# Kernel tuning notes

Measured on AMD Instinct MI355X. Metric: run time of the kernel, lower is better.

## Reference

```python
import jax, jax.numpy as jnp
import numpy as np

N = 4096   # number of observations
Q = 1024   # number of spatial locations (dist_matrix side)


def setup_inputs() -> dict:
    key = jax.random.key(0)
    k1, k2, k3, k4 = jax.random.split(key, 4)
    y_true = jax.random.normal(k1, (N, 1), dtype=jnp.float32)
    y_pred = jax.random.normal(k2, (N, 1), dtype=jnp.float32)
    Z_idx = jax.random.randint(k3, (N, 1), 0, Q).astype(jnp.int64)
    # symmetric distance matrix from random 2D coordinates
    coords = jax.random.uniform(k4, (Q, 2), dtype=jnp.float32) * 10.0
    diff = coords[:, None, :] - coords[None, :, :]
    dist_matrix = jnp.sqrt(jnp.sum(diff * diff, axis=-1) + 1e-12)
    sig2e = jnp.asarray(1.0, dtype=jnp.float32)
    sig2bs = jnp.ones((2,), dtype=jnp.float32)
    return {"y_true": y_true, "y_pred": y_pred, "Z_idx": Z_idx,
            "dist_matrix": dist_matrix, "sig2e": sig2e, "sig2bs": sig2bs}


def reference(y_true, y_pred, Z_idx, dist_matrix, sig2e, sig2bs):
    # NLL for the 'spatial' mixed-effects mode (custom_loss_lm).
    # V = sig2e*I + Z D Z^T with Z the one-hot indicator of Z_idx and
    # D[a,b] = sig2bs[0]*exp(-dist[a,b]/(2*sig2bs[1])).
    # Z D Z^T for one-hot Z is simply the row/col gather D[idx][:, idx],
    # which avoids materializing the dense N x Q indicator matrix.
    n = y_true.shape[0]
    idx = Z_idx[:, 0]
    D = sig2bs[0] * jnp.exp(-dist_matrix / (2.0 * sig2bs[1]))   # (Q, Q)
    V = sig2e * jnp.eye(n, dtype=jnp.float32) + D[idx][:, idx]  # (N, N)
    r = y_true - y_pred                                          # (N, 1)
    V_inv_r = jnp.linalg.solve(V, r)                             # (N, 1)
    quad = jnp.sum(r * V_inv_r)
    _, logdet = jnp.linalg.slogdet(V)
    log2pi = jnp.asarray(np.log(2.0 * np.pi), dtype=jnp.float32)
    total_loss = 0.5 * n * log2pi + 0.5 * logdet + 0.5 * quad
    return total_loss
```

## Files before the change

kernel.cpp:

```cpp
#include <hip/hip_runtime.h>
#include <math.h>

#define NN 4096
#define QQ 1024
#define LDA 1032
#define AF (1025 * 1032)


__device__ __forceinline__ void potrf64_run(float (&x)[16], int i, int q,
                                            float2 (&col2)[2][64]) {
#pragma unroll
    for (int qk = 0; qk < 4; ++qk) {
#pragma unroll
        for (int c2 = 0; c2 < 8; ++c2) {
            const int k = qk * 16 + 2 * c2;
            const int ck = 2 * c2;
            const int b = c2 & 1;
            if (q == qk) {
                float xk = x[ck];
                float d0 = __shfl(xk, k, 64);
                float rs0 = rsqrtf(d0);
                float l0 = (i == k) ? d0 * rs0 : xk * rs0;
                if (i >= k) x[ck] = l0;
                float lk1 = __shfl(l0, k + 1, 64);
                float x1v = fmaf(-l0, lk1, x[ck + 1]);
                float d1 = __shfl(x1v, k + 1, 64);
                float rs1 = rsqrtf(d1);
                float l1 = (i == k + 1) ? d1 * rs1 : x1v * rs1;
                if (i >= k + 1) x[ck + 1] = l1;
                col2[b][i] = make_float2(l0, l1);
            }
            __syncthreads();
            if (16 * q + 15 > k + 1 && i > k) {
                float2 lp = col2[b][i];
                const float4* cp = (const float4*)(&col2[b][16 * q]);
#pragma unroll
                for (int m2 = 0; m2 < 8; ++m2) {
                    float4 v = cp[m2];
                    if (16 * q + 2 * m2 > k + 1)
                        x[2 * m2] = fmaf(-lp.x, v.x, fmaf(-lp.y, v.y, x[2 * m2]));
                    if (16 * q + 2 * m2 + 1 > k + 1)
                        x[2 * m2 + 1] = fmaf(-lp.x, v.z, fmaf(-lp.y, v.w, x[2 * m2 + 1]));
                }
            }
        }
    }
}

template<bool DUAL>
__device__ __forceinline__ void trsm64_fused(float* Tr, float* Tc,
                                             const float (&Lb)[64][65],
                                             const float (&dinv)[64],
                                             float2 (&colr)[2][64],
                                             float2 (&colc)[2][64]) {
    const int tid = threadIdx.x;
    const int r = tid & 63, q = tid >> 6;
    float* tpr = Tr + r * 68 + 16 * q;
    float* tpc = Tc + r * 68 + 16 * q;
    float xr[16], xc[16];
#pragma unroll
    for (int m4 = 0; m4 < 4; ++m4) {
        float4 v = ((const float4*)tpr)[m4];
        xr[4 * m4] = v.x; xr[4 * m4 + 1] = v.y; xr[4 * m4 + 2] = v.z; xr[4 * m4 + 3] = v.w;
        if (DUAL) {
            float4 u = ((const float4*)tpc)[m4];
            xc[4 * m4] = u.x; xc[4 * m4 + 1] = u.y; xc[4 * m4 + 2] = u.z; xc[4 * m4 + 3] = u.w;
        }
    }
    float dv[16], ls[8];
#pragma unroll
    for (int m = 0; m < 16; ++m) dv[m] = dinv[16 * q + m];
#pragma unroll
    for (int c2 = 0; c2 < 8; ++c2) ls[c2] = Lb[16 * q + 2 * c2 + 1][16 * q + 2 * c2];
#pragma unroll
    for (int qk = 0; qk < 4; ++qk) {
#pragma unroll
        for (int c2 = 0; c2 < 8; ++c2) {
            const int k = qk * 16 + 2 * c2;
            const int ck = 2 * c2;
            const int b = c2 & 1;
            if (q == qk) {
                float l0 = xr[ck] * dv[ck];
                xr[ck] = l0;
                float l1 = fmaf(-l0, ls[c2], xr[ck + 1]) * dv[ck + 1];
                xr[ck + 1] = l1;
                colr[b][r] = make_float2(l0, l1);
                if (DUAL) {
                    float m0 = xc[ck] * dv[ck];
                    xc[ck] = m0;
                    float m1 = fmaf(-m0, ls[c2], xc[ck + 1]) * dv[ck + 1];
                    xc[ck + 1] = m1;
                    colc[b][r] = make_float2(m0, m1);
                }
            }
            __syncthreads();
            if (16 * q + 15 > k + 1) {
                float2 lr = colr[b][r];
                float2 lc;
                if (DUAL) lc = colc[b][r];
#pragma unroll
                for (int m2 = 0; m2 < 8; ++m2) {
                    const int c0 = 16 * q + 2 * m2;
                    if (c0 > k + 1) {
                        float a0 = Lb[c0][k], a1 = Lb[c0][k + 1];
                        xr[2 * m2] = fmaf(-lr.x, a0, fmaf(-lr.y, a1, xr[2 * m2]));
                        if (DUAL)
                            xc[2 * m2] = fmaf(-lc.x, a0, fmaf(-lc.y, a1, xc[2 * m2]));
                    }
                    if (c0 + 1 > k + 1) {
                        float b0 = Lb[c0 + 1][k], b1 = Lb[c0 + 1][k + 1];
                        xr[2 * m2 + 1] = fmaf(-lr.x, b0, fmaf(-lr.y, b1, xr[2 * m2 + 1]));
                        if (DUAL)
                            xc[2 * m2 + 1] = fmaf(-lc.x, b0, fmaf(-lc.y, b1, xc[2 * m2 + 1]));
                    }
                }
            }
        }
    }
#pragma unroll
    for (int m4 = 0; m4 < 4; ++m4) {
        ((float4*)tpr)[m4] = make_float4(xr[4 * m4], xr[4 * m4 + 1],
                                         xr[4 * m4 + 2], xr[4 * m4 + 3]);
        if (DUAL)
            ((float4*)tpc)[m4] = make_float4(xc[4 * m4], xc[4 * m4 + 1],
                                             xc[4 * m4 + 2], xc[4 * m4 + 3]);
    }
    __syncthreads();
}

__device__ __forceinline__ void panel_tile(
    float* __restrict__ A, float* __restrict__ scal, int p, int by, int bx,
    int nr, int ncol, float (&PrRaw)[64 * 68], float (&PcRaw)[64 * 68],
    float2 (&col2)[2][64], float2 (&colc)[2][64],
    float (&Lb)[64][65], float (&dinv)[64]) {
    const int tid = threadIdx.x;
    const int lane = tid & 63, wid = tid >> 6;
    int t0v = (p + 1) * 64;
    int r0 = t0v + by * 64;
    int c0 = t0v + bx * 64;
    bool wrow = (by == nr - 1);
    bool same_rc = (bx == by) && !wrow;
    bool dfuse = (bx == 0 && by == 0);
    int pc0 = p * 64;
    const float* db = A + (size_t)pc0 * (LDA + 1);
    for (int idx2 = tid; idx2 < 1024; idx2 += 256) {
        int rr = idx2 >> 4, c4 = idx2 & 15;
        int gr = r0 + rr;
        float4 v = make_float4(0.f, 0.f, 0.f, 0.f);
        if (gr <= QQ) v = *(const float4*)(A + (size_t)gr * LDA + pc0 + 4 * c4);
        *(float4*)(PrRaw + rr * 68 + 4 * c4) = v;
        if (!same_rc) {
            float4 u = *(const float4*)(A + (size_t)(c0 + rr) * LDA + pc0 + 4 * c4);
            *(float4*)(PcRaw + rr * 68 + 4 * c4) = u;
        }
    }
    for (int kk = tid; kk < 4096; kk += 256) {
        int ii = kk >> 6, jj = kk & 63;
        Lb[ii][jj] = db[(size_t)ii * LDA + jj];
    }
    if (tid < 64) dinv[tid] = 1.0f / db[(size_t)tid * (LDA + 1)];
    __syncthreads();
    if (same_rc) trsm64_fused<false>(PrRaw, PcRaw, Lb, dinv, col2, colc);
    else         trsm64_fused<true >(PrRaw, PcRaw, Lb, dinv, col2, colc);
    if (wrow && bx == 0 && wid == 0) {
        float xv = PrRaw[lane];
        float v = xv * xv;
        for (int o = 32; o > 0; o >>= 1) v += __shfl_down(v, o, 64);
        if (lane == 0) atomicAdd(&scal[2], v);
    }
    const float* PB = same_rc ? PrRaw : PcRaw;
    int tx = tid & 15, ty = tid >> 4;
    float acc[4][4];
#pragma unroll
    for (int ii = 0; ii < 4; ++ii)
#pragma unroll
        for (int jj = 0; jj < 4; ++jj) acc[ii][jj] = 0.f;
    float4 ar4[4], br4[4];
#pragma unroll 4
    for (int k4 = 0; k4 < 16; ++k4) {
#pragma unroll
        for (int ii = 0; ii < 4; ++ii)
            ar4[ii] = *(const float4*)(PrRaw + (ty + 16 * ii) * 68 + 4 * k4);
#pragma unroll
        for (int jj = 0; jj < 4; ++jj)
            br4[jj] = *(const float4*)(PB + (tx + 16 * jj) * 68 + 4 * k4);
#pragma unroll
        for (int ii = 0; ii < 4; ++ii)
#pragma unroll
            for (int jj = 0; jj < 4; ++jj) {
                acc[ii][jj] = fmaf(ar4[ii].x, br4[jj].x, acc[ii][jj]);
                acc[ii][jj] = fmaf(ar4[ii].y, br4[jj].y, acc[ii][jj]);
                acc[ii][jj] = fmaf(ar4[ii].z, br4[jj].z, acc[ii][jj]);
                acc[ii][jj] = fmaf(ar4[ii].w, br4[jj].w, acc[ii][jj]);
            }
    }
    if (!dfuse) {
#pragma unroll
        for (int ii = 0; ii < 4; ++ii) {
            int rr = r0 + ty + 16 * ii;
            if (rr <= QQ) {
#pragma unroll
                for (int jj = 0; jj < 4; ++jj) {
                    float* pa = A + (size_t)rr * LDA + c0 + tx + 16 * jj;
                    *pa -= acc[ii][jj];
                }
            }
        }
    } else {
#pragma unroll
        for (int ii = 0; ii < 4; ++ii) {
            int lr = ty + 16 * ii;
#pragma unroll
            for (int jj = 0; jj < 4; ++jj) {
                int lc = tx + 16 * jj;
                float old = A[(size_t)(r0 + lr) * LDA + c0 + lc];
                PcRaw[lr * 65 + lc] = old - acc[ii][jj];
            }
        }
        __syncthreads();
        int i = tid & 63, q = tid >> 6;
        float x[16];
#pragma unroll
        for (int m = 0; m < 16; ++m) x[m] = PcRaw[i * 65 + 16 * q + m];
        potrf64_run(x, i, q, col2);
        float* row = A + (size_t)(r0 + i) * LDA + c0 + 16 * q;
#pragma unroll
        for (int m4 = 0; m4 < 4; ++m4)
            ((float4*)row)[m4] = make_float4(x[4 * m4], x[4 * m4 + 1],
                                             x[4 * m4 + 2], x[4 * m4 + 3]);
    }
}

__global__ __launch_bounds__(256) void k_front(
    const float* __restrict__ yt, const float* __restrict__ yp,
    const int* __restrict__ idx, const float* __restrict__ dist,
    const float* __restrict__ se_p, const float* __restrict__ sbs,
    float* __restrict__ A, float* __restrict__ scal) {
    const int bid = blockIdx.x, tid = threadIdx.x;
    const int lane = tid & 63, wid = tid >> 6;
    __shared__ int   c_l[1024];
    __shared__ float s_l[1024];
    __shared__ float sq_l[1024];
    __shared__ __align__(16) float Pc[64 * 65];
    __shared__ float2 col2[2][64];
    __shared__ float red[4];
    float sb0 = sbs[0];
    float inv2 = 1.0f / (2.0f * sbs[1]);
    float inv_se = 1.0f / se_p[0];
    bool mv = (bid >= 128);

    for (int j = tid; j < 1024; j += 256) { c_l[j] = 0; s_l[j] = 0.f; }
    __syncthreads();
    float rr_acc = 0.f;
#pragma unroll
    for (int e4 = 0; e4 < 16; ++e4) {
        int e = tid + 256 * e4;
        int q = idx[e];
        atomicAdd(&c_l[q], 1);
        if (mv) {
            float r = yt[e] - yp[e];
            atomicAdd(&s_l[q], r);
            rr_acc += r * r;
        }
    }
    __syncthreads();
    for (int j = tid; j < 1024; j += 256) sq_l[j] = sqrtf((float)c_l[j]);
    __syncthreads();

    if (bid == 0) {
        for (int kk = tid; kk < 4096; kk += 256) {
            int i = kk >> 6, j = kk & 63;
            float qi = sq_l[i] * inv_se * sb0;
            Pc[i * 65 + j] = ((i == j) ? 1.0f : 0.0f)
                           + qi * sq_l[j] * __expf(-dist[(size_t)i * QQ + j] * inv2);
        }
        __syncthreads();
        int i = lane, q = wid;
        float x[16];
#pragma unroll
        for (int m = 0; m < 16; ++m) x[m] = Pc[i * 65 + 16 * q + m];
        potrf64_run(x, i, q, col2);
        float* row = A + (size_t)i * LDA + 16 * q;
#pragma unroll
        for (int m4 = 0; m4 < 4; ++m4)
            ((float4*)row)[m4] = make_float4(x[4 * m4], x[4 * m4 + 1],
                                             x[4 * m4 + 2], x[4 * m4 + 3]);
        if (tid == 0) scal[2] = 0.f;
    } else if (!mv) {
        for (int i = 64 + (bid - 1); i < QQ; i += 127) {
            float qi = sq_l[i] * inv_se * sb0;
            float4 d = ((const float4*)(dist + (size_t)i * QQ))[tid];
            int j0 = 4 * tid;
            float4 o;
            o.x = ((i == j0    ) ? 1.0f : 0.0f) + qi * sq_l[j0    ] * __expf(-d.x * inv2);
            o.y = ((i == j0 + 1) ? 1.0f : 0.0f) + qi * sq_l[j0 + 1] * __expf(-d.y * inv2);
            o.z = ((i == j0 + 2) ? 1.0f : 0.0f) + qi * sq_l[j0 + 2] * __expf(-d.z * inv2);
            o.w = ((i == j0 + 3) ? 1.0f : 0.0f) + qi * sq_l[j0 + 3] * __expf(-d.w * inv2);
            ((float4*)(A + (size_t)i * LDA))[tid] = o;
        }
    } else {
        int m = bid - 128;
        if (bid == 128) {
            float v = rr_acc;
            for (int o = 32; o > 0; o >>= 1) v += __shfl_down(v, o, 64);
            if (lane == 0) red[wid] = v;
            __syncthreads();
            if (tid == 0) scal[0] = red[0] + red[1] + red[2] + red[3];
            __syncthreads();
        }
        float st_acc = 0.f;
#pragma unroll
        for (int h = 0; h < 2; ++h) {
            int row = m * 8 + wid * 2 + h;
            const float* dr = dist + (size_t)row * QQ;
            float acc = 0.f;
#pragma unroll
            for (int j4 = 0; j4 < 16; ++j4) {
                int j = lane + 64 * j4;
                acc += __expf(-dr[j] * inv2) * s_l[j];
            }
            for (int o = 32; o > 0; o >>= 1) acc += __shfl_down(acc, o, 64);
            if (lane == 0) {
                float tv = acc * sb0;
                A[(size_t)QQ * LDA + row] = sq_l[row] * tv;
                st_acc += s_l[row] * tv;
            }
        }
        __syncthreads();
        if (lane == 0) red[wid] = st_acc;
        __syncthreads();
        if (tid == 0) scal[16 + m] = red[0] + red[1] + red[2] + red[3];
    }
}

__global__ __launch_bounds__(256) void k_panel(float* __restrict__ A,
                                               float* __restrict__ scal, int p) {
    __shared__ __align__(16) float PrRaw[64 * 68];
    __shared__ __align__(16) float PcRaw[64 * 68];
    __shared__ float2 col2[2][64];
    __shared__ float2 colc[2][64];
    __shared__ float Lb[64][65];
    __shared__ float dinv[64];
    int t0v = (p + 1) * 64;
    int rows = (QQ + 1) - t0v;
    int nr = (rows + 63) >> 6;
    int ncol = (QQ - t0v) / 64;
    int by = -1, bx = 0, rem = blockIdx.x;
    for (int b = 0; b < nr; ++b) {
        int cn = (b + 1 < ncol) ? (b + 1) : ncol;
        if (cn < 1) cn = 1;
        if (rem < cn) { by = b; bx = rem; break; }
        rem -= cn;
    }
    if (by < 0) return;
    panel_tile(A, scal, p, by, bx, nr, ncol, PrRaw, PcRaw, col2, colc, Lb, dinv);
}

__global__ __launch_bounds__(256) void k_final(float* __restrict__ A,
                                               float* __restrict__ scal,
                                               const float* __restrict__ se_p,
                                               float* __restrict__ out) {
    const int tid = threadIdx.x;
    const int lane = tid & 63, wid = tid >> 6;
    __shared__ float Lb[64][65];
    __shared__ float r1s[4], r2s[4], r3s[4];
    __shared__ float wl[64];
    const float* db15 = A + (size_t)960 * LDA + 960;
    for (int kk = tid; kk < 4096; kk += 256) {
        int ii = kk >> 6, jj = kk & 63;
        Lb[ii][jj] = db15[(size_t)ii * LDA + jj];
    }
    __syncthreads();
    if (tid < 64) {
        float xv = A[(size_t)QQ * LDA + 960 + tid];
        for (int k = 0; k < 64; ++k) {
            if (tid == k) xv /= Lb[k][k];
            float xk = __shfl(xv, k, 64);
            if (tid > k) xv = fmaf(-Lb[tid][k], xk, xv);
        }
        wl[tid] = xv;
    }
    __syncthreads();
    float v1 = 0.f, v2 = 0.f;
    for (int i = tid; i < QQ; i += 256) {
        v1 += __logf(A[(size_t)i * LDA + i]);
        if (i >= 960) { float yv = wl[i - 960]; v2 += yv * yv; }
    }
    v1 *= 2.0f;
    float v3 = (tid < 128) ? scal[16 + tid] : 0.f;
    for (int o = 32; o > 0; o >>= 1) {
        v1 += __shfl_down(v1, o, 64);
        v2 += __shfl_down(v2, o, 64);
        v3 += __shfl_down(v3, o, 64);
    }
    if (lane == 0) { r1s[wid] = v1; r2s[wid] = v2; r3s[wid] = v3; }
    __syncthreads();
    if (tid == 0) {
        float ld = r1s[0] + r1s[1] + r1s[2] + r1s[3];
        float wsq = __hip_atomic_load(&scal[2], __ATOMIC_RELAXED, __HIP_MEMORY_SCOPE_AGENT);
        float yy = r2s[0] + r2s[1] + r2s[2] + r2s[3] + wsq;
        float st = r3s[0] + r3s[1] + r3s[2] + r3s[3];
        float se = se_p[0], inv = 1.0f / se;
        float rr = scal[0];
        float quad = rr * inv - inv * inv * (st - inv * yy);
        float logdetV = (float)NN * __logf(se) + ld;
        out[0] = 0.5f * (float)NN * 1.8378770664093453f + 0.5f * logdetV + 0.5f * quad;
    }
}

extern "C" void kernel_launch(void* const* d_in, const int* in_sizes, int n_in,
                              void* d_out, int out_size, void* d_ws, size_t ws_size,
                              hipStream_t stream) {
    const float* yt   = (const float*)d_in[0];
    const float* yp   = (const float*)d_in[1];
    const int*   idx  = (const int*)d_in[2];
    const float* dist = (const float*)d_in[3];
    const float* se   = (const float*)d_in[4];
    const float* sbs  = (const float*)d_in[5];
    float* out = (float*)d_out;

    float* W    = (float*)d_ws;
    float* A    = W;
    float* scal = W + AF;

    k_front<<<dim3(256), dim3(256), 0, stream>>>(yt, yp, idx, dist, se, sbs, A, scal);
    for (int p = 0; p <= 14; ++p) {
        int t0v = (p + 1) * 64;
        int nr = ((QQ + 1) - t0v + 63) / 64;
        int ncol = (QQ - t0v) / 64;
        int tiles = 0;
        for (int b = 0; b < nr; ++b) {
            int cn = (b + 1 < ncol) ? (b + 1) : ncol;
            if (cn < 1) cn = 1;
            tiles += cn;
        }
        k_panel<<<dim3(tiles), dim3(256), 0, stream>>>(A, scal, p);
    }
    k_final<<<dim3(1), dim3(256), 0, stream>>>(A, scal, se, out);
}
```

Before: 786.4 us.

## Fuse two blocked Cholesky panel steps into one kernel launch

```diff
diff --git a/kernel.cpp b/kernel.cpp
--- a/kernel.cpp
+++ b/kernel.cpp
@@ -126,6 +126,197 @@
                                              xc[4 * m4 + 2], xc[4 * m4 + 3]);
     }
     __syncthreads();
+}
+
+__device__ __forceinline__ void stage68(float* Bf, const float* __restrict__ A,
+                                        int rb, int cb) {
+    for (int idx2 = threadIdx.x; idx2 < 1024; idx2 += 256) {
+        int rr = idx2 >> 4, c4 = idx2 & 15;
+        int gr = rb + rr;
+        float4 v = make_float4(0.f, 0.f, 0.f, 0.f);
+        if (gr <= QQ) v = *(const float4*)(A + (size_t)gr * LDA + cb + 4 * c4);
+        *(float4*)(Bf + rr * 68 + 4 * c4) = v;
+    }
+}
+
+template<int LDD>
+__device__ __forceinline__ void gemm_sub(float* D, const float* U, const float* V) {
+    int tx = threadIdx.x & 15, ty = threadIdx.x >> 4;
+    float a[4][4];
+#pragma unroll
+    for (int ii = 0; ii < 4; ++ii)
+#pragma unroll
+        for (int jj = 0; jj < 4; ++jj) a[ii][jj] = 0.f;
+    float4 ar4[4], br4[4];
+#pragma unroll 4
+    for (int k4 = 0; k4 < 16; ++k4) {
+#pragma unroll
+        for (int ii = 0; ii < 4; ++ii)
+            ar4[ii] = *(const float4*)(U + (ty + 16 * ii) * 68 + 4 * k4);
+#pragma unroll
+        for (int jj = 0; jj < 4; ++jj)
+            br4[jj] = *(const float4*)(V + (tx + 16 * jj) * 68 + 4 * k4);
+#pragma unroll
+        for (int ii = 0; ii < 4; ++ii)
+#pragma unroll
+            for (int jj = 0; jj < 4; ++jj) {
+                a[ii][jj] = fmaf(ar4[ii].x, br4[jj].x, a[ii][jj]);
+                a[ii][jj] = fmaf(ar4[ii].y, br4[jj].y, a[ii][jj]);
+                a[ii][jj] = fmaf(ar4[ii].z, br4[jj].z, a[ii][jj]);
+                a[ii][jj] = fmaf(ar4[ii].w, br4[jj].w, a[ii][jj]);
+            }
+    }
+#pragma unroll
+    for (int ii = 0; ii < 4; ++ii)
+#pragma unroll
+        for (int jj = 0; jj < 4; ++jj)
+            D[(ty + 16 * ii) * LDD + tx + 16 * jj] -= a[ii][jj];
+}
+
+__device__ __forceinline__ void acc_syrk(float (&acc)[4][4], const float* U,
+                                         const float* V) {
+    int tx = threadIdx.x & 15, ty = threadIdx.x >> 4;
+    float4 ar4[4], br4[4];
+#pragma unroll 4
+    for (int k4 = 0; k4 < 16; ++k4) {
+#pragma unroll
+        for (int ii = 0; ii < 4; ++ii)
+            ar4[ii] = *(const float4*)(U + (ty + 16 * ii) * 68 + 4 * k4);
+#pragma unroll
+        for (int jj = 0; jj < 4; ++jj)
+            br4[jj] = *(const float4*)(V + (tx + 16 * jj) * 68 + 4 * k4);
+#pragma unroll
+        for (int ii = 0; ii < 4; ++ii)
+#pragma unroll
+            for (int jj = 0; jj < 4; ++jj) {
+                acc[ii][jj] = fmaf(ar4[ii].x, br4[jj].x, acc[ii][jj]);
+                acc[ii][jj] = fmaf(ar4[ii].y, br4[jj].y, acc[ii][jj]);
+                acc[ii][jj] = fmaf(ar4[ii].z, br4[jj].z, acc[ii][jj]);
+                acc[ii][jj] = fmaf(ar4[ii].w, br4[jj].w, acc[ii][jj]);
+            }
+    }
+}
+
+__global__ __launch_bounds__(256) void k_pair(float* __restrict__ A,
+                                              float* __restrict__ scal, int p) {
+    __shared__ float Lb[64][65];
+    __shared__ float dinvp[64], dinv1[64];
+    __shared__ float2 col2[2][64], colc[2][64];
+    __shared__ __align__(16) float B1[64 * 68];
+    __shared__ __align__(16) float B2[64 * 68];
+    __shared__ __align__(16) float B3[64 * 68];
+    __shared__ __align__(16) float B4[64 * 68];
+    const int tid = threadIdx.x;
+    const int lane = tid & 63, wid = tid >> 6;
+    const int pc0 = p * 64, t1 = pc0 + 64, t2 = pc0 + 128;
+    int rows2 = (QQ + 1) - t2;
+    int nr2 = (rows2 + 63) >> 6;
+    int ncol2 = (QQ - t2) / 64;
+    int by = -1, bx = 0, rem = blockIdx.x;
+    for (int b = 0; b < nr2; ++b) {
+        int cn = (b + 1 < ncol2) ? (b + 1) : ncol2;
+        if (rem < cn) { by = b; bx = rem; break; }
+        rem -= cn;
+    }
+    if (by < 0) return;
+    int r0 = t2 + by * 64;
+    int c0 = t2 + bx * 64;
+    bool wrow = (by == nr2 - 1);
+    bool same_rc = (bx == by) && !wrow;
+    bool dfuse = (bx == 0 && by == 0);
+
+    for (int kk = tid; kk < 4096; kk += 256)
+        Lb[kk >> 6][kk & 63] = A[(size_t)(pc0 + (kk >> 6)) * LDA + pc0 + (kk & 63)];
+    stage68(B1, A, t1, pc0);
+    stage68(B2, A, r0, pc0);
+    if (!same_rc) stage68(B3, A, c0, pc0);
+    __syncthreads();
+    if (tid < 64) dinvp[tid] = 1.0f / Lb[tid][tid];
+    __syncthreads();
+    trsm64_fused<true>(B1, B2, Lb, dinvp, col2, colc);
+    if (!same_rc) trsm64_fused<false>(B3, B3, Lb, dinvp, col2, colc);
+    if (wrow && bx == 0 && wid == 0) {
+        float xv = B2[lane];
+        float v = xv * xv;
+        for (int o = 32; o > 0; o >>= 1) v += __shfl_down(v, o, 64);
+        if (lane == 0) atomicAdd(&scal[2], v);
+    }
+    float acc[4][4];
+#pragma unroll
+    for (int ii = 0; ii < 4; ++ii)
+#pragma unroll
+        for (int jj = 0; jj < 4; ++jj) acc[ii][jj] = 0.f;
+    acc_syrk(acc, B2, same_rc ? B2 : B3);
+    __syncthreads();
+    for (int kk = tid; kk < 4096; kk += 256)
+        Lb[kk >> 6][kk & 63] = A[(size_t)(t1 + (kk >> 6)) * LDA + t1 + (kk & 63)];
+    __syncthreads();
+    gemm_sub<65>(&Lb[0][0], B1, B1);
+    __syncthreads();
+    {
+        int i = lane, q = wid;
+        float x[16];
+#pragma unroll
+        for (int m = 0; m < 16; ++m) x[m] = Lb[i][16 * q + m];
+        potrf64_run(x, i, q, col2);
+#pragma unroll
+        for (int m = 0; m < 16; ++m) Lb[i][16 * q + m] = x[m];
+    }
+    __syncthreads();
+    if (tid < 64) dinv1[tid] = 1.0f / Lb[tid][tid];
+    stage68(B4, A, r0, t1);
+    __syncthreads();
+    gemm_sub<68>(B4, B2, B1);
+    __syncthreads();
+    if (!same_rc) {
+        stage68(B2, A, c0, t1);
+        __syncthreads();
+        gemm_sub<68>(B2, B3, B1);
+        __syncthreads();
+    }
+    if (same_rc) trsm64_fused<false>(B4, B4, Lb, dinv1, col2, colc);
+    else         trsm64_fused<true >(B4, B2, Lb, dinv1, col2, colc);
+    if (wrow && bx == 0 && wid == 0) {
+        float xv = B4[lane];
+        float v = xv * xv;
+        for (int o = 32; o > 0; o >>= 1) v += __shfl_down(v, o, 64);
+        if (lane == 0) atomicAdd(&scal[2], v);
+    }
+    acc_syrk(acc, B4, same_rc ? B4 : B2);
+    int tx = tid & 15, ty = tid >> 4;
+    if (!dfuse) {
+#pragma unroll
+        for (int ii = 0; ii < 4; ++ii) {
+            int rr = r0 + ty + 16 * ii;
+            if (rr <= QQ) {
+#pragma unroll
+                for (int jj = 0; jj < 4; ++jj)
+                    A[(size_t)rr * LDA + c0 + tx + 16 * jj] -= acc[ii][jj];
+            }
+        }
+    } else {
+        __syncthreads();
+        for (int kk = tid; kk < 4096; kk += 256)
+            A[(size_t)(t1 + (kk >> 6)) * LDA + t1 + (kk & 63)] = Lb[kk >> 6][kk & 63];
+        __syncthreads();
+#pragma unroll
+        for (int ii = 0; ii < 4; ++ii)
+#pragma unroll
+            for (int jj = 0; jj < 4; ++jj)
+                Lb[ty + 16 * ii][tx + 16 * jj] =
+                    A[(size_t)(t2 + ty + 16 * ii) * LDA + t2 + tx + 16 * jj] - acc[ii][jj];
+        __syncthreads();
+        int i = lane, q = wid;
+        float x[16];
+#pragma unroll
+        for (int m = 0; m < 16; ++m) x[m] = Lb[i][16 * q + m];
+        potrf64_run(x, i, q, col2);
+        float* row = A + (size_t)(t2 + i) * LDA + t2 + 16 * q;
+#pragma unroll
+        for (int m4 = 0; m4 < 4; ++m4)
+            ((float4*)row)[m4] = make_float4(x[4 * m4], x[4 * m4 + 1],
+                                             x[4 * m4 + 2], x[4 * m4 + 3]);
+    }
 }
 
 __device__ __forceinline__ void panel_tile(
@@ -175,35 +366,15 @@
     for (int ii = 0; ii < 4; ++ii)
 #pragma unroll
         for (int jj = 0; jj < 4; ++jj) acc[ii][jj] = 0.f;
-    float4 ar4[4], br4[4];
-#pragma unroll 4
-    for (int k4 = 0; k4 < 16; ++k4) {
-#pragma unroll
-        for (int ii = 0; ii < 4; ++ii)
-            ar4[ii] = *(const float4*)(PrRaw + (ty + 16 * ii) * 68 + 4 * k4);
-#pragma unroll
-        for (int jj = 0; jj < 4; ++jj)
-            br4[jj] = *(const float4*)(PB + (tx + 16 * jj) * 68 + 4 * k4);
-#pragma unroll
-        for (int ii = 0; ii < 4; ++ii)
-#pragma unroll
-            for (int jj = 0; jj < 4; ++jj) {
-                acc[ii][jj] = fmaf(ar4[ii].x, br4[jj].x, acc[ii][jj]);
-                acc[ii][jj] = fmaf(ar4[ii].y, br4[jj].y, acc[ii][jj]);
-                acc[ii][jj] = fmaf(ar4[ii].z, br4[jj].z, acc[ii][jj]);
-                acc[ii][jj] = fmaf(ar4[ii].w, br4[jj].w, acc[ii][jj]);
-            }
-    }
+    acc_syrk(acc, PrRaw, PB);
     if (!dfuse) {
 #pragma unroll
         for (int ii = 0; ii < 4; ++ii) {
             int rr = r0 + ty + 16 * ii;
             if (rr <= QQ) {
 #pragma unroll
-                for (int jj = 0; jj < 4; ++jj) {
-                    float* pa = A + (size_t)rr * LDA + c0 + tx + 16 * jj;
-                    *pa -= acc[ii][jj];
-                }
+                for (int jj = 0; jj < 4; ++jj)
+                    A[(size_t)rr * LDA + c0 + tx + 16 * jj] -= acc[ii][jj];
             }
         }
     } else {
@@ -424,7 +595,17 @@
     float* scal = W + AF;
 
     k_front<<<dim3(256), dim3(256), 0, stream>>>(yt, yp, idx, dist, se, sbs, A, scal);
-    for (int p = 0; p <= 14; ++p) {
+    for (int p = 0; p <= 12; p += 2) {
+        int t2 = (p + 2) * 64;
+        int nr2 = ((QQ + 1) - t2 + 63) / 64;
+        int ncol2 = (QQ - t2) / 64;
+        int tiles = 0;
+        for (int b = 0; b < nr2; ++b)
+            tiles += (b + 1 < ncol2) ? (b + 1) : ncol2;
+        k_pair<<<dim3(tiles), dim3(256), 0, stream>>>(A, scal, p);
+    }
+    {
+        int p = 14;
         int t0v = (p + 1) * 64;
         int nr = ((QQ + 1) - t0v + 63) / 64;
         int ncol = (QQ - t0v) / 64;
```

Result: slower. 1.019 ms (+29.6%).
